# Kernel optimization log

Hardware: AMD Instinct MI355X
Metric: run time of the kernel (lower is better)

## Reference

```python
import jax, jax.numpy as jnp
import numpy as np

B, S, H = 128, 256, 512


def setup_inputs() -> dict:
    key = jax.random.key(0)
    ks = jax.random.split(key, 20)
    sc = 0.02
    inp = {
        "facts": jax.random.normal(ks[0], (B, S, H), jnp.float32),
        "questions": jax.random.normal(ks[1], (B, 1, H), jnp.float32),
        "prevM": jax.random.normal(ks[2], (B, 1, H), jnp.float32),
        # interaction gate MLP: z1 (4H->H), z2 (H->1)
        "z1_w": jax.random.normal(ks[3], (4 * H, H), jnp.float32) * sc,
        "z1_b": jnp.zeros((H,), jnp.float32),
        "z2_w": jax.random.normal(ks[4], (H, 1), jnp.float32) * sc,
        "z2_b": jnp.zeros((1,), jnp.float32),
        # AttentionGRUCell params (input_size = hidden_size = H)
        "Wr": jax.random.normal(ks[5], (H, H), jnp.float32) * sc,
        "br": jnp.zeros((H,), jnp.float32),
        "Ur": jax.random.normal(ks[6], (H, H), jnp.float32) * sc,
        "bur": jnp.zeros((H,), jnp.float32),
        "W": jax.random.normal(ks[7], (H, H), jnp.float32) * sc,
        "bw": jnp.zeros((H,), jnp.float32),
        "U": jax.random.normal(ks[8], (H, H), jnp.float32) * sc,
        "bu": jnp.zeros((H,), jnp.float32),
        # next memory projection (3H -> H)
        "nm_w": jax.random.normal(ks[9], (3 * H, H), jnp.float32) * sc,
        "nm_b": jnp.zeros((H,), jnp.float32),
    }
    return inp


def _episodic_memory(facts, questions, prevM,
                     z1_w, z1_b, z2_w, z2_b,
                     Wr, br, Ur, bur, W, bw, U, bu,
                     nm_w, nm_b):
    # ---- make_interaction ----
    q = questions  # (B,1,H) broadcasts against (B,S,H)
    m = prevM
    z = jnp.concatenate(
        [facts * q, facts * m, jnp.abs(facts - q), jnp.abs(facts - m)],
        axis=2,
    )  # (B,S,4H)
    g_hidden = jnp.tanh(jnp.einsum("bsf,fh->bsh", z, z1_w) + z1_b)
    G_logits = (jnp.einsum("bsh,ho->bso", g_hidden, z2_w) + z2_b)[..., 0]  # (B,S)
    G = jax.nn.softmax(G_logits, axis=1)  # (B,S)

    # ---- AttentionGRU scan over sentences ----
    pre_r = jnp.einsum("bsh,hk->bsh", facts, Wr) + br  # Wr @ fact, all steps
    pre_h = jnp.einsum("bsh,hk->bsh", facts, W) + bw   # W  @ fact, all steps

    def step(C, xs):
        pr, ph, g = xs  # (B,H), (B,H), (B,)
        r = jax.nn.sigmoid(pr + C @ Ur + bur)
        h_tilda = jnp.tanh(ph + r * (C @ U + bu))
        g = g[:, None]
        return g * h_tilda + (1.0 - g) * C, None

    C0 = jnp.zeros((facts.shape[0], Wr.shape[1]), facts.dtype)
    xs = (jnp.swapaxes(pre_r, 0, 1), jnp.swapaxes(pre_h, 0, 1), G.T)  # lead S
    C, _ = jax.lax.scan(step, C0, xs)  # (B,H)

    # ---- next memory ----
    concat = jnp.concatenate([prevM[:, 0], C, questions[:, 0]], axis=1)  # (B,3H)
    next_mem = jax.nn.relu(concat @ nm_w + nm_b)
    return next_mem[:, None, :]  # (B,1,H)


def reference(facts, questions, prevM, z1_w, z1_b, z2_w, z2_b,
              Wr, br, Ur, bur, W, bw, U, bu, nm_w, nm_b):
    return _episodic_memory(facts, questions, prevM, z1_w, z1_b, z2_w, z2_b,
                            Wr, br, Ur, bur, W, bw, U, bu, nm_w, nm_b)
```

## Files before the change

### kernel.cpp

```cpp
#include <hip/hip_runtime.h>
#include <stdint.h>

#define B_ 128
#define S_ 256
#define H_ 512

typedef __attribute__((ext_vector_type(4))) float f32x4;
typedef __attribute__((ext_vector_type(4))) int i32x4;
typedef __attribute__((ext_vector_type(2))) unsigned int u32x2;
typedef __attribute__((ext_vector_type(8))) __bf16 bf16x8;
typedef unsigned long long u64;

#define OFF_G      0
#define OFF_RSR    131072
#define OFF_RSH    133120
#define OFF_FLG    135168
#define OFF_EX     139264
#define OFF_CBUF   401408
#define OFF_BP     663552
#define OFF_PB     2760704
#define OFF_LOGITS 3809280

__device__ __forceinline__ unsigned short f2bf(float f) {
  unsigned u = __builtin_bit_cast(unsigned, f);
  u += 0x7FFFu + ((u >> 16) & 1u);
  return (unsigned short)(u >> 16);
}
__device__ __forceinline__ float fast_sigmoid(float x) {
  return 1.0f / (1.0f + __expf(-x));
}
__device__ __forceinline__ float fast_tanh(float x) {
  return 1.0f - 2.0f / (__expf(2.0f * x) + 1.0f);
}

__global__ void k_prep_bp(const float* __restrict__ z1w,
                          unsigned short* __restrict__ Bp) {
  int t = blockIdx.x * blockDim.x + threadIdx.x;
  int k = t >> 9, n = t & 511;
  Bp[((k >> 3) * 512 + n) * 8 + (k & 7)] = f2bf(z1w[t]);
}

__global__ void k_prep_pb(const float* __restrict__ Ur,
                          const float* __restrict__ U,
                          unsigned short* __restrict__ PB) {
  int t = blockIdx.x * blockDim.x + threadIdx.x;
  int j = t & 7;
  int l = (t >> 3) & 63;
  int kt = (t >> 9) & 15;
  int mat = (t >> 13) & 1;
  int w = (t >> 14) & 7;
  int mem = t >> 17;
  int k = kt * 32 + ((l >> 4) & 3) * 8 + j;
  int n = mem * 128 + w * 16 + (l & 15);
  const float* src = mat ? U : Ur;
  PB[t] = f2bf(src[k * 512 + n]);
}

__global__ void k_prep_rs(const float* __restrict__ Wr,
                          const float* __restrict__ W,
                          float* __restrict__ rsr, float* __restrict__ rsh) {
  __shared__ float red[4];
  int h2 = blockIdx.x;
  int t = threadIdx.x;
  const float* M = (h2 >= 512) ? W : Wr;
  int h = h2 & 511;
  float sv = M[h * 512 + t] + M[h * 512 + 256 + t];
#pragma unroll
  for (int mask = 1; mask < 64; mask <<= 1) sv += __shfl_xor(sv, mask, 64);
  if ((t & 63) == 0) red[t >> 6] = sv;
  __syncthreads();
  if (t == 0) {
    float tot = red[0] + red[1] + red[2] + red[3];
    ((h2 >= 512) ? rsh : rsr)[h] = tot;
  }
}

__global__ __launch_bounds__(512, 4) void k_gate(
    const float* __restrict__ facts, const float* __restrict__ questions,
    const float* __restrict__ prevM, const float* __restrict__ z1b,
    const float* __restrict__ z2w, const unsigned short* __restrict__ Bp,
    float* __restrict__ logits) {
  __shared__ float qS[512], mS[512], z1bS[512], z2wS[512];
  __shared__ unsigned short At[64 * 40];
  __shared__ unsigned short Bt[16384];
  __shared__ float lp[64 * 4];
  const int tid = threadIdx.x;
  const int row0 = blockIdx.x * 64;
  const int b = row0 >> 8;
  const int s0 = row0 & 255;
  qS[tid] = questions[b * 512 + tid];
  mS[tid] = prevM[b * 512 + tid];
  z1bS[tid] = z1b[tid];
  z2wS[tid] = z2w[tid];
  const int w = tid >> 6, l = tid & 63;
  const int mgrp = w & 1, ngrp = w >> 1;
  const int lm = l & 15, lk = l >> 4;
  f32x4 acc[2][8];
#pragma unroll
  for (int a = 0; a < 2; ++a)
#pragma unroll
    for (int i = 0; i < 8; ++i) acc[a][i] = (f32x4){0.f, 0.f, 0.f, 0.f};
  const int arow = tid >> 3, ac = tid & 7;
  const float* fbase = facts + ((size_t)(b * 256 + s0 + arow)) * 512 + ac * 4;

  for (int kb = 0; kb < 64; ++kb) {
    __syncthreads();
    {
      const char* gsrc = (const char*)Bp + (size_t)kb * 32768 + w * 4096 + l * 16;
#pragma unroll
      for (int i = 0; i < 4; ++i)
        __builtin_amdgcn_global_load_lds(
            (const __attribute__((address_space(1))) unsigned int*)(gsrc +
                                                                    i * 1024),
            (__attribute__((address_space(3))) unsigned int*)((char*)Bt +
                                                              w * 4096 +
                                                              i * 1024),
            16, 0, 0);
    }
    const int part = kb >> 4;
    const int h0 = (kb & 15) * 32;
    f32x4 fv = *(const f32x4*)(fbase + h0);
    f32x4 ov = (part & 1) ? *(const f32x4*)&mS[h0 + ac * 4]
                          : *(const f32x4*)&qS[h0 + ac * 4];
    float z0, z1, z2, z3;
    if (part < 2) {
      z0 = fv[0] * ov[0]; z1 = fv[1] * ov[1];
      z2 = fv[2] * ov[2]; z3 = fv[3] * ov[3];
    } else {
      z0 = fabsf(fv[0] - ov[0]); z1 = fabsf(fv[1] - ov[1]);
      z2 = fabsf(fv[2] - ov[2]); z3 = fabsf(fv[3] - ov[3]);
    }
    unsigned p0 = (unsigned)f2bf(z0) | ((unsigned)f2bf(z1) << 16);
    unsigned p1 = (unsigned)f2bf(z2) | ((unsigned)f2bf(z3) << 16);
    u32x2 pk = {p0, p1};
    *(u32x2*)&At[arow * 40 + ac * 4] = pk;
    __syncthreads();
    bf16x8 af[2];
#pragma unroll
    for (int mi = 0; mi < 2; ++mi) {
      i32x4 av = *(const i32x4*)&At[((mgrp * 2 + mi) * 16 + lm) * 40 + lk * 8];
      af[mi] = __builtin_bit_cast(bf16x8, av);
    }
#pragma unroll
    for (int i = 0; i < 8; ++i) {
      const int nt = ngrp * 8 + i;
      i32x4 bv = *(const i32x4*)&Bt[lk * 4096 + (nt * 16 + lm) * 8];
      bf16x8 bf = __builtin_bit_cast(bf16x8, bv);
      acc[0][i] = __builtin_amdgcn_mfma_f32_16x16x32_bf16(af[0], bf, acc[0][i], 0, 0, 0);
      acc[1][i] = __builtin_amdgcn_mfma_f32_16x16x32_bf16(af[1], bf, acc[1][i], 0, 0, 0);
    }
  }
  float pr_[2][4];
#pragma unroll
  for (int mi = 0; mi < 2; ++mi)
#pragma unroll
    for (int r = 0; r < 4; ++r) pr_[mi][r] = 0.f;
#pragma unroll
  for (int i = 0; i < 8; ++i) {
    const int n_i = (ngrp * 8 + i) * 16 + lm;
    const float zb = z1bS[n_i], zw = z2wS[n_i];
#pragma unroll
    for (int mi = 0; mi < 2; ++mi)
#pragma unroll
      for (int r = 0; r < 4; ++r)
        pr_[mi][r] += fast_tanh(acc[mi][i][r] + zb) * zw;
  }
#pragma unroll
  for (int mask = 1; mask < 16; mask <<= 1)
#pragma unroll
    for (int mi = 0; mi < 2; ++mi)
#pragma unroll
      for (int r = 0; r < 4; ++r)
        pr_[mi][r] += __shfl_xor(pr_[mi][r], mask, 64);
  if (lm == 0) {
#pragma unroll
    for (int mi = 0; mi < 2; ++mi)
#pragma unroll
      for (int r = 0; r < 4; ++r)
        lp[((mgrp * 2 + mi) * 16 + lk * 4 + r) * 4 + ngrp] = pr_[mi][r];
  }
  __syncthreads();
  if (tid < 64)
    logits[row0 + tid] =
        lp[tid * 4] + lp[tid * 4 + 1] + lp[tid * 4 + 2] + lp[tid * 4 + 3];
}

__global__ void k_softmax(const float* __restrict__ logits,
                          float* __restrict__ GT) {
  __shared__ float red[4], red2[4];
  int b = blockIdx.x, t = threadIdx.x;
  float v = logits[b * 256 + t];
  float mx = v;
#pragma unroll
  for (int mask = 1; mask < 64; mask <<= 1)
    mx = fmaxf(mx, __shfl_xor(mx, mask, 64));
  if ((t & 63) == 0) red[t >> 6] = mx;
  __syncthreads();
  mx = fmaxf(fmaxf(red[0], red[1]), fmaxf(red[2], red[3]));
  float e = __expf(v - mx);
  float sm = e;
#pragma unroll
  for (int mask = 1; mask < 64; mask <<= 1) sm += __shfl_xor(sm, mask, 64);
  if ((t & 63) == 0) red2[t >> 6] = sm;
  __syncthreads();
  sm = red2[0] + red2[1] + red2[2] + red2[3];
  GT[t * 128 + b] = e / sm;
}

__global__ __launch_bounds__(512, 1) void k_scan(
    const float* __restrict__ facts, const float* __restrict__ GT,
    const unsigned short* __restrict__ PB, const float* __restrict__ rsr,
    const float* __restrict__ rsh, const float* __restrict__ br,
    const float* __restrict__ bur, const float* __restrict__ bw,
    const float* __restrict__ bu, unsigned int* __restrict__ EX,
    unsigned int* __restrict__ FLG, float* __restrict__ Cb) {
  __shared__ unsigned short A[16 * 520];
  const int tid = threadIdx.x;
  const int g = blockIdx.x & 7;
  const int mem = blockIdx.x >> 3;
  const int w = tid >> 6, l = tid & 63;
  const int lm = l & 15, lk = (l >> 4) & 3;
  for (int i = tid; i < 16 * 520 / 4; i += 512) ((u64*)A)[i] = 0ull;
  i32x4 bfr[2][16];
  const char* pb = (const char*)PB + (size_t)(mem * 8 + w) * 32768;
#pragma unroll
  for (int mat = 0; mat < 2; ++mat)
#pragma unroll
    for (int kt = 0; kt < 16; ++kt)
      bfr[mat][kt] = *(const i32x4*)(pb + (mat * 16 + kt) * 1024 + l * 16);
  const int n = mem * 128 + w * 16 + lm;
  const int b0 = g * 16 + lk * 4;
  const float c_rsr = rsr[n], c_br = br[n];
  const float c_rsh = rsh[n], c_bw = bw[n];
  const float c_bur = bur[n], c_bu = bu[n];
  const float* fb[4];
#pragma unroll
  for (int r = 0; r < 4; ++r)
    fb[r] = facts + (size_t)(b0 + r) * (256 * 512) + n;
  const int grow = tid >> 5, gcu = tid & 31;
  const u64* EXQ = (const u64*)EX;
  f32x4 Cv = (f32x4){0.f, 0.f, 0.f, 0.f};
  float fct[4];
#pragma unroll
  for (int r = 0; r < 4; ++r) fct[r] = fb[r][0];
  f32x4 gvv = *(const f32x4*)(GT + b0);
  __syncthreads();

  for (int s = 0; s < 256; ++s) {
    const unsigned tag = (unsigned)(s + 1);
    const unsigned rbase = ((unsigned)(s & 1) * 8 + (unsigned)g) * 16;
    f32x4 acc0 = (f32x4){0.f, 0.f, 0.f, 0.f};
    f32x4 acc1 = (f32x4){0.f, 0.f, 0.f, 0.f};
#pragma unroll
    for (int kt = 0; kt < 16; ++kt) {
      i32x4 av = *(const i32x4*)&A[lm * 520 + kt * 32 + lk * 8];
      bf16x8 afv = __builtin_bit_cast(bf16x8, av);
      acc0 = __builtin_amdgcn_mfma_f32_16x16x32_bf16(
          afv, __builtin_bit_cast(bf16x8, bfr[0][kt]), acc0, 0, 0, 0);
      acc1 = __builtin_amdgcn_mfma_f32_16x16x32_bf16(
          afv, __builtin_bit_cast(bf16x8, bfr[1][kt]), acc1, 0, 0, 0);
    }
    unsigned pkd[4];
#pragma unroll
    for (int r = 0; r < 4; ++r) {
      const float pr = fct[r] * c_rsr + c_br;
      const float ph = fct[r] * c_rsh + c_bw;
      const float r_ = fast_sigmoid(pr + acc0[r] + c_bur);
      const float ht = fast_tanh(ph + r_ * (acc1[r] + c_bu));
      Cv[r] = gvv[r] * ht + (1.0f - gvv[r]) * Cv[r];
      const int mb = (int)f2bf(Cv[r]);
      pkd[r] = (unsigned)mb | ((unsigned)__shfl_xor(mb, 1, 64) << 16);
    }
    if (!(lm & 1)) {
#pragma unroll
      for (int r = 0; r < 4; ++r)
        __hip_atomic_store(EX + (rbase + (unsigned)(lk * 4 + r)) * 256 +
                               ((unsigned)n >> 1),
                           pkd[r], __ATOMIC_RELAXED, __HIP_MEMORY_SCOPE_AGENT);
    }
    float fctn[4];
    f32x4 gvn = gvv;
    if (s < 255) {
#pragma unroll
      for (int r = 0; r < 4; ++r) fctn[r] = fb[r][(size_t)(s + 1) * 512];
      gvn = *(const f32x4*)(GT + (s + 1) * 128 + b0);
    } else {
#pragma unroll
      for (int r = 0; r < 4; ++r) fctn[r] = 0.f;
    }
    __syncthreads();
    if (tid == 0)
      __hip_atomic_store(FLG + g * 4 + mem, tag, __ATOMIC_RELAXED,
                         __HIP_MEMORY_SCOPE_AGENT);
    if (!(lm & 1)) {
#pragma unroll
      for (int r = 0; r < 4; ++r)
        *(unsigned*)((char*)A + (lk * 4 + r) * 1040 + n * 2) = pkd[r];
    }
    {
#pragma unroll
      for (int j = 0; j < 3; ++j) {
        const int q = j + (j >= mem ? 1 : 0);
        int guard = 0;
        while (__hip_atomic_load(FLG + g * 4 + q, __ATOMIC_RELAXED,
                                 __HIP_MEMORY_SCOPE_AGENT) < tag) {
          __builtin_amdgcn_s_sleep(1);
          if (++guard > (1 << 22)) break;
        }
      }
      u64 wv[3];
#pragma unroll
      for (int j = 0; j < 3; ++j) {
        const int q = j + (j >= mem ? 1 : 0);
        wv[j] = __hip_atomic_load(
            EXQ + (rbase + (unsigned)grow) * 128 + (unsigned)(q * 32 + gcu),
            __ATOMIC_RELAXED, __HIP_MEMORY_SCOPE_AGENT);
      }
#pragma unroll
      for (int j = 0; j < 3; ++j) {
        const int q = j + (j >= mem ? 1 : 0);
        *(u64*)((char*)A + grow * 1040 + q * 256 + gcu * 8) = wv[j];
      }
    }
    __syncthreads();
#pragma unroll
    for (int r = 0; r < 4; ++r) fct[r] = fctn[r];
    gvv = gvn;
  }
#pragma unroll
  for (int r = 0; r < 4; ++r) Cb[(size_t)(b0 + r) * 512 + n] = Cv[r];
}

__global__ __launch_bounds__(512) void k_final(
    const float* __restrict__ prevM, const float* __restrict__ questions,
    const float* __restrict__ Cb, const float* __restrict__ nmw,
    const float* __restrict__ nmb, float* __restrict__ out) {
  __shared__ float cc[2][1536];
  const int t = threadIdx.x;
  const int b0 = blockIdx.x * 2;
  for (int i = t; i < 1536; i += 512) {
#pragma unroll
    for (int bi = 0; bi < 2; ++bi) {
      int bbx = b0 + bi;
      float v;
      if (i < 512) v = prevM[bbx * 512 + i];
      else if (i < 1024) v = Cb[bbx * 512 + i - 512];
      else v = questions[bbx * 512 + i - 1024];
      cc[bi][i] = v;
    }
  }
  __syncthreads();
  const int h = t;
  float a0 = nmb[h], a1 = nmb[h];
#pragma unroll 4
  for (int f = 0; f < 1536; ++f) {
    float wv = nmw[f * 512 + h];
    a0 = fmaf(cc[0][f], wv, a0);
    a1 = fmaf(cc[1][f], wv, a1);
  }
  out[(size_t)b0 * 512 + h] = fmaxf(a0, 0.f);
  out[(size_t)(b0 + 1) * 512 + h] = fmaxf(a1, 0.f);
}

extern "C" void kernel_launch(void* const* d_in, const int* in_sizes, int n_in,
                              void* d_out, int out_size, void* d_ws,
                              size_t ws_size, hipStream_t stream) {
  const float* facts     = (const float*)d_in[0];
  const float* questions = (const float*)d_in[1];
  const float* prevM     = (const float*)d_in[2];
  const float* z1w       = (const float*)d_in[3];
  const float* z1b       = (const float*)d_in[4];
  const float* z2w       = (const float*)d_in[5];
  const float* Wr        = (const float*)d_in[7];
  const float* br        = (const float*)d_in[8];
  const float* Ur        = (const float*)d_in[9];
  const float* bur       = (const float*)d_in[10];
  const float* W         = (const float*)d_in[11];
  const float* bw        = (const float*)d_in[12];
  const float* U         = (const float*)d_in[13];
  const float* bu        = (const float*)d_in[14];
  const float* nmw       = (const float*)d_in[15];
  const float* nmb       = (const float*)d_in[16];

  char* ws = (char*)d_ws;
  float* GT            = (float*)(ws + OFF_G);
  float* rsr           = (float*)(ws + OFF_RSR);
  float* rsh           = (float*)(ws + OFF_RSH);
  unsigned* FLG        = (unsigned*)(ws + OFF_FLG);
  unsigned* EX         = (unsigned*)(ws + OFF_EX);
  float* Cb            = (float*)(ws + OFF_CBUF);
  float* logits        = (float*)(ws + OFF_LOGITS);
  unsigned short* Bp   = (unsigned short*)(ws + OFF_BP);
  unsigned short* PB   = (unsigned short*)(ws + OFF_PB);

  hipMemsetAsync(FLG, 0, 32 * sizeof(unsigned), stream);
  k_prep_bp<<<2048, 512, 0, stream>>>(z1w, Bp);
  k_prep_pb<<<1024, 512, 0, stream>>>(Ur, U, PB);
  k_prep_rs<<<1024, 256, 0, stream>>>(Wr, W, rsr, rsh);
  k_gate<<<512, 512, 0, stream>>>(facts, questions, prevM, z1b, z2w, Bp, logits);
  k_softmax<<<128, 256, 0, stream>>>(logits, GT);
  k_scan<<<32, 512, 0, stream>>>(facts, GT, PB, rsr, rsh, br, bur, bw, bu, EX,
                                 FLG, Cb);
  k_final<<<64, 512, 0, stream>>>(prevM, questions, Cb, nmw, nmb, (float*)d_out);
}
```

Measured before the change: 1.121 ms.

## Enlarge gate GEMM row tile, fuse prep kernels, batch four rows in final

The gate GEMM now processes 128 rows per block instead of 64. Each wave covers 16 N-tiles, so every staged block of the bf16 weight is reused across twice as many rows and global traffic for the weight is halved; the cost is a larger accumulator footprint and fewer resident blocks. The three weight-preparation kernels are merged into one launch to cut launch overhead. The final projection handles four batch rows per block so each weight load is reused four times.

```diff
diff --git a/kernel.cpp b/kernel.cpp
--- a/kernel.cpp
+++ b/kernel.cpp
@@ -33,75 +33,77 @@
   return 1.0f - 2.0f / (__expf(2.0f * x) + 1.0f);
 }
 
-__global__ void k_prep_bp(const float* __restrict__ z1w,
-                          unsigned short* __restrict__ Bp) {
-  int t = blockIdx.x * blockDim.x + threadIdx.x;
-  int k = t >> 9, n = t & 511;
-  Bp[((k >> 3) * 512 + n) * 8 + (k & 7)] = f2bf(z1w[t]);
-}
-
-__global__ void k_prep_pb(const float* __restrict__ Ur,
-                          const float* __restrict__ U,
-                          unsigned short* __restrict__ PB) {
-  int t = blockIdx.x * blockDim.x + threadIdx.x;
-  int j = t & 7;
-  int l = (t >> 3) & 63;
-  int kt = (t >> 9) & 15;
-  int mat = (t >> 13) & 1;
-  int w = (t >> 14) & 7;
-  int mem = t >> 17;
-  int k = kt * 32 + ((l >> 4) & 3) * 8 + j;
-  int n = mem * 128 + w * 16 + (l & 15);
-  const float* src = mat ? U : Ur;
-  PB[t] = f2bf(src[k * 512 + n]);
-}
-
-__global__ void k_prep_rs(const float* __restrict__ Wr,
-                          const float* __restrict__ W,
-                          float* __restrict__ rsr, float* __restrict__ rsh) {
-  __shared__ float red[4];
-  int h2 = blockIdx.x;
-  int t = threadIdx.x;
-  const float* M = (h2 >= 512) ? W : Wr;
-  int h = h2 & 511;
-  float sv = M[h * 512 + t] + M[h * 512 + 256 + t];
-#pragma unroll
-  for (int mask = 1; mask < 64; mask <<= 1) sv += __shfl_xor(sv, mask, 64);
-  if ((t & 63) == 0) red[t >> 6] = sv;
-  __syncthreads();
-  if (t == 0) {
-    float tot = red[0] + red[1] + red[2] + red[3];
-    ((h2 >= 512) ? rsh : rsr)[h] = tot;
-  }
-}
-
-__global__ __launch_bounds__(512, 4) void k_gate(
+__global__ __launch_bounds__(512) void k_prep(
+    const float* __restrict__ z1w, const float* __restrict__ Ur,
+    const float* __restrict__ U, const float* __restrict__ Wr,
+    const float* __restrict__ W, unsigned short* __restrict__ Bp,
+    unsigned short* __restrict__ PB, float* __restrict__ rsr,
+    float* __restrict__ rsh) {
+  __shared__ float red[8];
+  const int blk = blockIdx.x, tid = threadIdx.x;
+  if (blk < 2048) {
+    int t = blk * 512 + tid;
+    int k = t >> 9, n = t & 511;
+    Bp[((k >> 3) * 512 + n) * 8 + (k & 7)] = f2bf(z1w[t]);
+  } else if (blk < 3072) {
+    int t = (blk - 2048) * 512 + tid;
+    int j = t & 7;
+    int l = (t >> 3) & 63;
+    int kt = (t >> 9) & 15;
+    int mat = (t >> 13) & 1;
+    int w = (t >> 14) & 7;
+    int mem = t >> 17;
+    int k = kt * 32 + ((l >> 4) & 3) * 8 + j;
+    int n = mem * 128 + w * 16 + (l & 15);
+    const float* src = mat ? U : Ur;
+    PB[t] = f2bf(src[k * 512 + n]);
+  } else {
+    int h2 = (blk - 3072) * 2 + (tid >> 8);
+    int t2 = tid & 255;
+    const float* M = (h2 >= 512) ? W : Wr;
+    int h = h2 & 511;
+    float sv = M[h * 512 + t2] + M[h * 512 + 256 + t2];
+#pragma unroll
+    for (int mask = 1; mask < 64; mask <<= 1) sv += __shfl_xor(sv, mask, 64);
+    if ((tid & 63) == 0) red[tid >> 6] = sv;
+    __syncthreads();
+    if (tid == 0) {
+      float tot = red[0] + red[1] + red[2] + red[3];
+      ((h2 >= 512) ? rsh : rsr)[h] = tot;
+    } else if (tid == 256) {
+      float tot = red[4] + red[5] + red[6] + red[7];
+      int h2b = h2;
+      ((h2b >= 512) ? rsh : rsr)[h2b & 511] = tot;
+    }
+  }
+}
+
+__global__ __launch_bounds__(512, 2) void k_gate(
     const float* __restrict__ facts, const float* __restrict__ questions,
     const float* __restrict__ prevM, const float* __restrict__ z1b,
     const float* __restrict__ z2w, const unsigned short* __restrict__ Bp,
     float* __restrict__ logits) {
   __shared__ float qS[512], mS[512], z1bS[512], z2wS[512];
-  __shared__ unsigned short At[64 * 40];
+  __shared__ unsigned short At[128 * 40];
   __shared__ unsigned short Bt[16384];
-  __shared__ float lp[64 * 4];
+  __shared__ float lp[128 * 2];
   const int tid = threadIdx.x;
-  const int row0 = blockIdx.x * 64;
+  const int row0 = blockIdx.x * 128;
   const int b = row0 >> 8;
-  const int s0 = row0 & 255;
   qS[tid] = questions[b * 512 + tid];
   mS[tid] = prevM[b * 512 + tid];
   z1bS[tid] = z1b[tid];
   z2wS[tid] = z2w[tid];
   const int w = tid >> 6, l = tid & 63;
-  const int mgrp = w & 1, ngrp = w >> 1;
+  const int mgrp = w & 3, ngrp = w >> 2;
   const int lm = l & 15, lk = l >> 4;
-  f32x4 acc[2][8];
+  f32x4 acc[2][16];
 #pragma unroll
   for (int a = 0; a < 2; ++a)
 #pragma unroll
-    for (int i = 0; i < 8; ++i) acc[a][i] = (f32x4){0.f, 0.f, 0.f, 0.f};
-  const int arow = tid >> 3, ac = tid & 7;
-  const float* fbase = facts + ((size_t)(b * 256 + s0 + arow)) * 512 + ac * 4;
+    for (int i = 0; i < 16; ++i) acc[a][i] = (f32x4){0.f, 0.f, 0.f, 0.f};
+  const int arow = tid >> 2, ac = tid & 3;
+  const float* fbase = facts + (size_t)(row0 + arow) * 512 + ac * 8;
 
   for (int kb = 0; kb < 64; ++kb) {
     __syncthreads();
@@ -119,21 +121,36 @@
     }
     const int part = kb >> 4;
     const int h0 = (kb & 15) * 32;
-    f32x4 fv = *(const f32x4*)(fbase + h0);
-    f32x4 ov = (part & 1) ? *(const f32x4*)&mS[h0 + ac * 4]
-                          : *(const f32x4*)&qS[h0 + ac * 4];
-    float z0, z1, z2, z3;
+    f32x4 fv0 = *(const f32x4*)(fbase + h0);
+    f32x4 fv1 = *(const f32x4*)(fbase + h0 + 4);
+    f32x4 ov0, ov1;
+    if (part & 1) {
+      ov0 = *(const f32x4*)&mS[h0 + ac * 8];
+      ov1 = *(const f32x4*)&mS[h0 + ac * 8 + 4];
+    } else {
+      ov0 = *(const f32x4*)&qS[h0 + ac * 8];
+      ov1 = *(const f32x4*)&qS[h0 + ac * 8 + 4];
+    }
+    float z[8];
     if (part < 2) {
-      z0 = fv[0] * ov[0]; z1 = fv[1] * ov[1];
-      z2 = fv[2] * ov[2]; z3 = fv[3] * ov[3];
+#pragma unroll
+      for (int i = 0; i < 4; ++i) {
+        z[i] = fv0[i] * ov0[i];
+        z[4 + i] = fv1[i] * ov1[i];
+      }
     } else {
-      z0 = fabsf(fv[0] - ov[0]); z1 = fabsf(fv[1] - ov[1]);
-      z2 = fabsf(fv[2] - ov[2]); z3 = fabsf(fv[3] - ov[3]);
-    }
-    unsigned p0 = (unsigned)f2bf(z0) | ((unsigned)f2bf(z1) << 16);
-    unsigned p1 = (unsigned)f2bf(z2) | ((unsigned)f2bf(z3) << 16);
-    u32x2 pk = {p0, p1};
-    *(u32x2*)&At[arow * 40 + ac * 4] = pk;
+#pragma unroll
+      for (int i = 0; i < 4; ++i) {
+        z[i] = fabsf(fv0[i] - ov0[i]);
+        z[4 + i] = fabsf(fv1[i] - ov1[i]);
+      }
+    }
+    i32x4 pk;
+#pragma unroll
+    for (int i = 0; i < 4; ++i)
+      pk[i] = (int)((unsigned)f2bf(z[2 * i]) |
+                    ((unsigned)f2bf(z[2 * i + 1]) << 16));
+    *(i32x4*)&At[arow * 40 + ac * 8] = pk;
     __syncthreads();
     bf16x8 af[2];
 #pragma unroll
@@ -142,8 +159,8 @@
       af[mi] = __builtin_bit_cast(bf16x8, av);
     }
 #pragma unroll
-    for (int i = 0; i < 8; ++i) {
-      const int nt = ngrp * 8 + i;
+    for (int i = 0; i < 16; ++i) {
+      const int nt = ngrp * 16 + i;
       i32x4 bv = *(const i32x4*)&Bt[lk * 4096 + (nt * 16 + lm) * 8];
       bf16x8 bf = __builtin_bit_cast(bf16x8, bv);
       acc[0][i] = __builtin_amdgcn_mfma_f32_16x16x32_bf16(af[0], bf, acc[0][i], 0, 0, 0);
@@ -156,8 +173,8 @@
 #pragma unroll
     for (int r = 0; r < 4; ++r) pr_[mi][r] = 0.f;
 #pragma unroll
-  for (int i = 0; i < 8; ++i) {
-    const int n_i = (ngrp * 8 + i) * 16 + lm;
+  for (int i = 0; i < 16; ++i) {
+    const int n_i = (ngrp * 16 + i) * 16 + lm;
     const float zb = z1bS[n_i], zw = z2wS[n_i];
 #pragma unroll
     for (int mi = 0; mi < 2; ++mi)
@@ -177,12 +194,10 @@
     for (int mi = 0; mi < 2; ++mi)
 #pragma unroll
       for (int r = 0; r < 4; ++r)
-        lp[((mgrp * 2 + mi) * 16 + lk * 4 + r) * 4 + ngrp] = pr_[mi][r];
+        lp[((mgrp * 2 + mi) * 16 + lk * 4 + r) * 2 + ngrp] = pr_[mi][r];
   }
   __syncthreads();
-  if (tid < 64)
-    logits[row0 + tid] =
-        lp[tid * 4] + lp[tid * 4 + 1] + lp[tid * 4 + 2] + lp[tid * 4 + 3];
+  if (tid < 128) logits[row0 + tid] = lp[tid * 2] + lp[tid * 2 + 1];
 }
 
 __global__ void k_softmax(const float* __restrict__ logits,
@@ -335,12 +350,12 @@
     const float* __restrict__ prevM, const float* __restrict__ questions,
     const float* __restrict__ Cb, const float* __restrict__ nmw,
     const float* __restrict__ nmb, float* __restrict__ out) {
-  __shared__ float cc[2][1536];
+  __shared__ float cc[4][1536];
   const int t = threadIdx.x;
-  const int b0 = blockIdx.x * 2;
+  const int b0 = blockIdx.x * 4;
   for (int i = t; i < 1536; i += 512) {
 #pragma unroll
-    for (int bi = 0; bi < 2; ++bi) {
+    for (int bi = 0; bi < 4; ++bi) {
       int bbx = b0 + bi;
       float v;
       if (i < 512) v = prevM[bbx * 512 + i];
@@ -351,15 +366,19 @@
   }
   __syncthreads();
   const int h = t;
-  float a0 = nmb[h], a1 = nmb[h];
+  float a0 = nmb[h], a1 = a0, a2 = a0, a3 = a0;
 #pragma unroll 4
   for (int f = 0; f < 1536; ++f) {
     float wv = nmw[f * 512 + h];
     a0 = fmaf(cc[0][f], wv, a0);
     a1 = fmaf(cc[1][f], wv, a1);
+    a2 = fmaf(cc[2][f], wv, a2);
+    a3 = fmaf(cc[3][f], wv, a3);
   }
   out[(size_t)b0 * 512 + h] = fmaxf(a0, 0.f);
   out[(size_t)(b0 + 1) * 512 + h] = fmaxf(a1, 0.f);
+  out[(size_t)(b0 + 2) * 512 + h] = fmaxf(a2, 0.f);
+  out[(size_t)(b0 + 3) * 512 + h] = fmaxf(a3, 0.f);
 }
 
 extern "C" void kernel_launch(void* const* d_in, const int* in_sizes, int n_in,
@@ -393,13 +412,11 @@
   unsigned short* Bp   = (unsigned short*)(ws + OFF_BP);
   unsigned short* PB   = (unsigned short*)(ws + OFF_PB);
 
-  hipMemsetAsync(FLG, 0, 32 * sizeof(unsigned), stream);
-  k_prep_bp<<<2048, 512, 0, stream>>>(z1w, Bp);
-  k_prep_pb<<<1024, 512, 0, stream>>>(Ur, U, PB);
-  k_prep_rs<<<1024, 256, 0, stream>>>(Wr, W, rsr, rsh);
-  k_gate<<<512, 512, 0, stream>>>(facts, questions, prevM, z1b, z2w, Bp, logits);
+  hipMemsetAsync(FLG, 0, 128, stream);
+  k_prep<<<3584, 512, 0, stream>>>(z1w, Ur, U, Wr, W, Bp, PB, rsr, rsh);
+  k_gate<<<256, 512, 0, stream>>>(facts, questions, prevM, z1b, z2w, Bp, logits);
   k_softmax<<<128, 256, 0, stream>>>(logits, GT);
   k_scan<<<32, 512, 0, stream>>>(facts, GT, PB, rsr, rsh, br, bur, bw, bu, EX,
                                  FLG, Cb);
-  k_final<<<64, 512, 0, stream>>>(prevM, questions, Cb, nmw, nmb, (float*)d_out);
-}
+  k_final<<<32, 512, 0, stream>>>(prevM, questions, Cb, nmw, nmb, (float*)d_out);
+}
```

Result: slower. 1.145 ms (+2.2%).
